# Kernel optimization log

Hardware: AMD Instinct MI355X
Metric: run time of the kernel (lower is better)

Reference implementation:

```python
import jax, jax.numpy as jnp
import numpy as np

LATENT_DIM = 16
POLY_ORDER = 3

# static index sets matching the ordering of the torch loops
_PAIR_I, _PAIR_J = np.triu_indices(LATENT_DIM)  # i<=j, row-major over i then j
_TRIPLES = np.array([(i, j, k)
                     for i in range(LATENT_DIM)
                     for j in range(i, LATENT_DIM)
                     for k in range(j, LATENT_DIM)], dtype=np.int32)
_TRI_I, _TRI_J, _TRI_K = _TRIPLES[:, 0], _TRIPLES[:, 1], _TRIPLES[:, 2]


def compute_library_order1(z):
    """Vectorized SINDy polynomial library: [1, z_i, z_i z_j (i<=j), z_i z_j z_k (i<=j<=k)]."""
    n = z.shape[0]
    ones = jnp.ones((n, 1), dtype=z.dtype)
    pairs = z[:, _PAIR_I] * z[:, _PAIR_J]                      # [N, 136]
    triples = z[:, _TRI_I] * z[:, _TRI_J] * z[:, _TRI_K]       # [N, 816]
    return jnp.concatenate([ones, z, pairs, triples], axis=1)  # [N, 969]


def setup_inputs() -> dict:
    key = jax.random.key(0)
    k1, k2 = jax.random.split(key)
    N = 262144
    library_dim = 1 + LATENT_DIM + _PAIR_I.shape[0] + _TRIPLES.shape[0]  # 969
    num_ode = 16
    z = jax.random.normal(k1, (N, LATENT_DIM), dtype=jnp.float32)
    coefficients = jax.random.normal(k2, (library_dim, num_ode), dtype=jnp.float32)
    coefficient_mask = jnp.ones((library_dim, num_ode), dtype=jnp.float32)
    return {"z": z, "coefficients": coefficients, "coefficient_mask": coefficient_mask}


def reference(z, coefficients, coefficient_mask):
    theta = compute_library_order1(z)                      # [N, 969]
    masked_coefficients = coefficients * coefficient_mask  # [969, 16]
    z_dot_pred = theta @ masked_coefficients               # [N, 16]
    l1_reg_loss = jnp.mean(jnp.abs(masked_coefficients))
    return (z_dot_pred, l1_reg_loss)
```

## Files before the change

### kernel.cpp

```cpp
#include <hip/hip_runtime.h>
#include <hip/hip_bf16.h>


#define LIB    969
#define NSLOT  248
#define NCHUNK 31
#define NROWS  262144
#define NOUT   16
#define BTAB_U4 1984

typedef __attribute__((ext_vector_type(8))) short bf16x8;
typedef __attribute__((ext_vector_type(4))) float f32x4;

struct Maps {
  unsigned char a[NSLOT], b[NSLOT], c[NSLOT];
  short l[NSLOT][4];
};

constexpr Maps build_maps() {
  Maps M{};
  int n = 0;
  M.a[n] = 16; M.b[n] = 16; M.c[n] = 16;
  M.l[n][0] = 0; M.l[n][1] = -1; M.l[n][2] = -1; M.l[n][3] = -1; n++;
  for (int a0 = 0; a0 < 4; a0++) {
    M.a[n] = (unsigned char)a0; M.b[n] = 16; M.c[n] = 16;
    for (int g = 0; g < 4; g++) M.l[n][g] = (short)(1 + ((a0 + 4 * g) & 15));
    n++;
  }
  bool pv[16][16] = {};
  for (int i = 0; i < 16; i++)
    for (int j = i; j < 16; j++) {
      if (pv[i][j]) continue;
      M.a[n] = (unsigned char)i; M.b[n] = (unsigned char)j; M.c[n] = 16;
      int mi[4], mj[4];
      for (int g = 0; g < 4; g++) {
        int x = (i + 4 * g) & 15, y = (j + 4 * g) & 15;
        int lo = x < y ? x : y, hi = x < y ? y : x;
        mi[g] = lo; mj[g] = hi; pv[lo][hi] = true;
      }
      for (int g = 0; g < 4; g++) {
        bool dup = false;
        for (int h = 0; h < g; h++) if (mi[h] == mi[g] && mj[h] == mj[g]) dup = true;
        M.l[n][g] = dup ? (short)-1
                        : (short)(17 + mi[g] * 16 - mi[g] * (mi[g] - 1) / 2 + (mj[g] - mi[g]));
      }
      n++;
    }
  bool tv[16][16][16] = {};
  for (int i = 0; i < 16; i++)
    for (int j = i; j < 16; j++)
      for (int k = j; k < 16; k++) {
        if (tv[i][j][k]) continue;
        M.a[n] = (unsigned char)i; M.b[n] = (unsigned char)j; M.c[n] = (unsigned char)k;
        int ti[4], tj[4], tk[4];
        for (int g = 0; g < 4; g++) {
          int x = (i + 4 * g) & 15, y = (j + 4 * g) & 15, w = (k + 4 * g) & 15, t;
          if (x > y) { t = x; x = y; y = t; }
          if (y > w) { t = y; y = w; w = t; }
          if (x > y) { t = x; x = y; y = t; }
          ti[g] = x; tj[g] = y; tk[g] = w; tv[x][y][w] = true;
        }
        for (int g = 0; g < 4; g++) {
          bool dup = false;
          for (int h = 0; h < g; h++)
            if (ti[h] == ti[g] && tj[h] == tj[g] && tk[h] == tk[g]) dup = true;
          if (dup) { M.l[n][g] = -1; continue; }
          int i2 = ti[g], j2 = tj[g], k2 = tk[g];
          int base = 0;
          for (int a2 = 0; a2 < i2; a2++) base += (16 - a2) * (17 - a2) / 2;
          int off = (j2 - i2) * (16 - i2) - (j2 - i2) * (j2 - i2 - 1) / 2 + (k2 - j2);
          M.l[n][g] = (short)(153 + base + off);
        }
        n++;
      }
  for (; n < NSLOT; n++) {
    M.a[n] = 16; M.b[n] = 16; M.c[n] = 16;
    M.l[n][0] = M.l[n][1] = M.l[n][2] = M.l[n][3] = -1;
  }
  return M;
}
constexpr Maps MP = build_maps();

__device__ inline unsigned short f2bf(float x) {
  unsigned int u = __builtin_bit_cast(unsigned int, x);
  u += 0x7fffu + ((u >> 16) & 1u);
  return (unsigned short)(u >> 16);
}
__global__ __launch_bounds__(256) void prep_kernel(const float* __restrict__ C,
                                                   const float* __restrict__ M,
                                                   unsigned short* __restrict__ Cb,
                                                   float* __restrict__ acc) {
  const int idx = blockIdx.x * 256 + threadIdx.x;
  const int s = idx >> 6, g = (idx >> 4) & 3, o = idx & 15;
  const int li = MP.l[s][g];
  float v = 0.f;
  if (li >= 0) v = C[li * 16 + o] * M[li * 16 + o];
  Cb[(((s >> 3) * 4 + g) * 16 + o) * 8 + (s & 7)] = f2bf(v);
  float t = fabsf(v);
  #pragma unroll
  for (int off = 32; off > 0; off >>= 1) t += __shfl_down(t, off);
  if ((threadIdx.x & 63) == 0) atomicAdd(acc, t);
}

__global__ __launch_bounds__(256) void sindy_kernel(const float* __restrict__ z,
                                                    const unsigned short* __restrict__ Cb,
                                                    const float* __restrict__ acc,
                                                    float* __restrict__ out) {
  __shared__ uint4 Blds[BTAB_U4];
  const int lane = threadIdx.x & 63;
  const int g = lane >> 4;
  const int o = lane & 15;
  const int rowBase = blockIdx.x * 64 + (threadIdx.x >> 6) * 16;
  const int r = rowBase + o;

  float z17[17];
  {
    const float4* z4 = (const float4*)z;
    #pragma unroll
    for (int c4 = 0; c4 < 4; c4++) {
      float4 v = z4[r * 4 + c4];
      z17[c4 * 4 + 0] = v.x; z17[c4 * 4 + 1] = v.y;
      z17[c4 * 4 + 2] = v.z; z17[c4 * 4 + 3] = v.w;
    }
    z17[16] = 1.0f;
  }

  {
    const uint4* src = (const uint4*)Cb;
    #pragma unroll
    for (int i = 0; i < 8; i++) {
      int e = i * 256 + threadIdx.x;
      if (e < BTAB_U4) Blds[e] = src[e];
    }
  }
  __syncthreads();

  const bool b0 = (g & 1) != 0, b1 = (g & 2) != 0;
  float t16[16], zr[17];
  #pragma unroll
  for (int m = 0; m < 16; m++) t16[m] = b0 ? z17[(m + 4) & 15] : z17[m];
  #pragma unroll
  for (int m = 0; m < 16; m++) zr[m] = b1 ? t16[(m + 8) & 15] : t16[m];
  zr[16] = 1.0f;

  const char* bbase = (const char*)Blds + lane * 16;

  f32x4 acc4 = {0.f, 0.f, 0.f, 0.f};
  #pragma unroll
  for (int c = 0; c < NCHUNK; c++) {
    bf16x8 af;
    #pragma unroll
    for (int m = 0; m < 8; m++) {
      const int s = c * 8 + m;
      float th = (zr[MP.a[s]] * zr[MP.b[s]]) * zr[MP.c[s]];
      __hip_bfloat16 h = __float2bfloat16(th);
      unsigned short u; __builtin_memcpy(&u, &h, 2);
      af[m] = (short)u;
    }
    bf16x8 bfrag = *(const bf16x8*)(bbase + c * 1024);
    acc4 = __builtin_amdgcn_mfma_f32_16x16x32_bf16(af, bfrag, acc4, 0, 0, 0);
  }

  #pragma unroll
  for (int p = 0; p < 4; p++)
    out[(rowBase + 4 * g + p) * 16 + o] = acc4[p];

  if (blockIdx.x == 0 && threadIdx.x == 0)
    out[NROWS * NOUT] = acc[0] * (1.0f / 15504.0f);
}

extern "C" void kernel_launch(void* const* d_in, const int* in_sizes, int n_in,
                              void* d_out, int out_size, void* d_ws, size_t ws_size,
                              hipStream_t stream) {
  const float* z = (const float*)d_in[0];
  const float* C = (const float*)d_in[1];
  const float* M = (const float*)d_in[2];
  float* out = (float*)d_out;
  float* acc = (float*)d_ws;
  unsigned short* Cb = (unsigned short*)((char*)d_ws + 64);

  (void)hipMemsetAsync(d_ws, 0, 4, stream);
  prep_kernel<<<NSLOT * 4 * 16 / 256, 256, 0, stream>>>(C, M, Cb, acc);
  sindy_kernel<<<NROWS / 64, 256, 0, stream>>>(z, Cb, acc, out);
}
```

Baseline: 56.00 us.

## Persistent-ish waves with z prefetch, fp16 MFMA, and memset-free L1 reduction

Removes the hipMemsetAsync and the atomic by having one extra block of the prep kernel compute the L1 mean directly into the output. Each wave now processes four 16-row tiles with software prefetch of the next z tile, which amortizes the LDS coefficient-table load over more rows using a 1024-block grid. Theta values are packed with cvt_pkrtz into fp16 and fed to the f16 MFMA instead of bf16 with manual rounding, cutting conversion instructions. The fp16 path may overflow for large cubic terms and uses round-toward-zero, which changes accuracy.

Measured after the change: 58.11 us. +3.8%, slower.

```diff
diff --git a/kernel.cpp b/kernel.cpp
--- a/kernel.cpp
+++ b/kernel.cpp
@@ -8,9 +8,12 @@
 #define NROWS  262144
 #define NOUT   16
 #define BTAB_U4 1984
-
-typedef __attribute__((ext_vector_type(8))) short bf16x8;
-typedef __attribute__((ext_vector_type(4))) float f32x4;
+#define TPW    4
+#define NBLK   1024
+
+typedef _Float16 f16x8 __attribute__((ext_vector_type(8)));
+typedef __fp16   h16x2 __attribute__((ext_vector_type(2)));
+typedef float    f32x4 __attribute__((ext_vector_type(4)));
 
 struct Maps {
   unsigned char a[NSLOT], b[NSLOT], c[NSLOT];
@@ -32,7 +35,7 @@
     for (int j = i; j < 16; j++) {
       if (pv[i][j]) continue;
       M.a[n] = (unsigned char)i; M.b[n] = (unsigned char)j; M.c[n] = 16;
-      int mi[4], mj[4];
+      int mi[4] = {}, mj[4] = {};
       for (int g = 0; g < 4; g++) {
         int x = (i + 4 * g) & 15, y = (j + 4 * g) & 15;
         int lo = x < y ? x : y, hi = x < y ? y : x;
@@ -52,9 +55,9 @@
       for (int k = j; k < 16; k++) {
         if (tv[i][j][k]) continue;
         M.a[n] = (unsigned char)i; M.b[n] = (unsigned char)j; M.c[n] = (unsigned char)k;
-        int ti[4], tj[4], tk[4];
+        int ti[4] = {}, tj[4] = {}, tk[4] = {};
         for (int g = 0; g < 4; g++) {
-          int x = (i + 4 * g) & 15, y = (j + 4 * g) & 15, w = (k + 4 * g) & 15, t;
+          int x = (i + 4 * g) & 15, y = (j + 4 * g) & 15, w = (k + 4 * g) & 15, t = 0;
           if (x > y) { t = x; x = y; y = t; }
           if (y > w) { t = y; y = w; w = t; }
           if (x > y) { t = x; x = y; y = t; }
@@ -81,92 +84,107 @@
 }
 constexpr Maps MP = build_maps();
 
-__device__ inline unsigned short f2bf(float x) {
-  unsigned int u = __builtin_bit_cast(unsigned int, x);
-  u += 0x7fffu + ((u >> 16) & 1u);
-  return (unsigned short)(u >> 16);
-}
 __global__ __launch_bounds__(256) void prep_kernel(const float* __restrict__ C,
                                                    const float* __restrict__ M,
                                                    unsigned short* __restrict__ Cb,
-                                                   float* __restrict__ acc) {
-  const int idx = blockIdx.x * 256 + threadIdx.x;
-  const int s = idx >> 6, g = (idx >> 4) & 3, o = idx & 15;
-  const int li = MP.l[s][g];
-  float v = 0.f;
-  if (li >= 0) v = C[li * 16 + o] * M[li * 16 + o];
-  Cb[(((s >> 3) * 4 + g) * 16 + o) * 8 + (s & 7)] = f2bf(v);
-  float t = fabsf(v);
-  #pragma unroll
-  for (int off = 32; off > 0; off >>= 1) t += __shfl_down(t, off);
-  if ((threadIdx.x & 63) == 0) atomicAdd(acc, t);
-}
-
-__global__ __launch_bounds__(256) void sindy_kernel(const float* __restrict__ z,
-                                                    const unsigned short* __restrict__ Cb,
-                                                    const float* __restrict__ acc,
-                                                    float* __restrict__ out) {
+                                                   float* __restrict__ out) {
+  if (blockIdx.x < 62) {
+    const int idx = blockIdx.x * 256 + threadIdx.x;
+    const int s = idx >> 6, g = (idx >> 4) & 3, o = idx & 15;
+    const int li = MP.l[s][g];
+    float v = 0.f;
+    if (li >= 0) v = C[li * 16 + o] * M[li * 16 + o];
+    _Float16 h = (_Float16)v;
+    unsigned short u; __builtin_memcpy(&u, &h, 2);
+    Cb[(((s >> 3) * 4 + g) * 16 + o) * 8 + (s & 7)] = u;
+  } else {
+    __shared__ float part[4];
+    float t = 0.f;
+    for (int i = threadIdx.x; i < LIB * 16; i += 256) t += fabsf(C[i] * M[i]);
+    #pragma unroll
+    for (int off = 32; off > 0; off >>= 1) t += __shfl_down(t, off);
+    if ((threadIdx.x & 63) == 0) part[threadIdx.x >> 6] = t;
+    __syncthreads();
+    if (threadIdx.x == 0)
+      out[NROWS * NOUT] = (part[0] + part[1] + part[2] + part[3]) * (1.0f / 15504.0f);
+  }
+}
+
+__global__ __launch_bounds__(256, 4) void sindy_kernel(const float* __restrict__ z,
+                                                       const unsigned short* __restrict__ Cb,
+                                                       float* __restrict__ out) {
   __shared__ uint4 Blds[BTAB_U4];
+  {
+    const uint4* src = (const uint4*)Cb;
+    #pragma unroll
+    for (int i = 0; i < 8; i++) {
+      int e = i * 256 + threadIdx.x;
+      if (e < BTAB_U4) Blds[e] = src[e];
+    }
+  }
+
   const int lane = threadIdx.x & 63;
   const int g = lane >> 4;
   const int o = lane & 15;
-  const int rowBase = blockIdx.x * 64 + (threadIdx.x >> 6) * 16;
-  const int r = rowBase + o;
-
-  float z17[17];
+  const int wid = blockIdx.x * 4 + (threadIdx.x >> 6);
+  const bool b0 = (g & 1) != 0, b1 = (g & 2) != 0;
+  const char* bbase = (const char*)Blds + lane * 16;
+
+  float4 zn[4];
   {
     const float4* z4 = (const float4*)z;
+    const int r = wid * TPW * 16 + o;
+    #pragma unroll
+    for (int c4 = 0; c4 < 4; c4++) zn[c4] = z4[r * 4 + c4];
+  }
+  __syncthreads();
+
+  int t = wid * TPW;
+  #pragma unroll
+  for (int k = 0; k < TPW; ++k, ++t) {
+    float z17[17];
     #pragma unroll
     for (int c4 = 0; c4 < 4; c4++) {
-      float4 v = z4[r * 4 + c4];
-      z17[c4 * 4 + 0] = v.x; z17[c4 * 4 + 1] = v.y;
-      z17[c4 * 4 + 2] = v.z; z17[c4 * 4 + 3] = v.w;
+      z17[c4 * 4 + 0] = zn[c4].x; z17[c4 * 4 + 1] = zn[c4].y;
+      z17[c4 * 4 + 2] = zn[c4].z; z17[c4 * 4 + 3] = zn[c4].w;
     }
     z17[16] = 1.0f;
-  }
-
-  {
-    const uint4* src = (const uint4*)Cb;
-    #pragma unroll
-    for (int i = 0; i < 8; i++) {
-      int e = i * 256 + threadIdx.x;
-      if (e < BTAB_U4) Blds[e] = src[e];
-    }
-  }
-  __syncthreads();
-
-  const bool b0 = (g & 1) != 0, b1 = (g & 2) != 0;
-  float t16[16], zr[17];
-  #pragma unroll
-  for (int m = 0; m < 16; m++) t16[m] = b0 ? z17[(m + 4) & 15] : z17[m];
-  #pragma unroll
-  for (int m = 0; m < 16; m++) zr[m] = b1 ? t16[(m + 8) & 15] : t16[m];
-  zr[16] = 1.0f;
-
-  const char* bbase = (const char*)Blds + lane * 16;
-
-  f32x4 acc4 = {0.f, 0.f, 0.f, 0.f};
-  #pragma unroll
-  for (int c = 0; c < NCHUNK; c++) {
-    bf16x8 af;
-    #pragma unroll
-    for (int m = 0; m < 8; m++) {
-      const int s = c * 8 + m;
-      float th = (zr[MP.a[s]] * zr[MP.b[s]]) * zr[MP.c[s]];
-      __hip_bfloat16 h = __float2bfloat16(th);
-      unsigned short u; __builtin_memcpy(&u, &h, 2);
-      af[m] = (short)u;
-    }
-    bf16x8 bfrag = *(const bf16x8*)(bbase + c * 1024);
-    acc4 = __builtin_amdgcn_mfma_f32_16x16x32_bf16(af, bfrag, acc4, 0, 0, 0);
-  }
-
-  #pragma unroll
-  for (int p = 0; p < 4; p++)
-    out[(rowBase + 4 * g + p) * 16 + o] = acc4[p];
-
-  if (blockIdx.x == 0 && threadIdx.x == 0)
-    out[NROWS * NOUT] = acc[0] * (1.0f / 15504.0f);
+    if (k + 1 < TPW) {
+      const float4* z4 = (const float4*)z;
+      const int r = (t + 1) * 16 + o;
+      #pragma unroll
+      for (int c4 = 0; c4 < 4; c4++) zn[c4] = z4[r * 4 + c4];
+    }
+    float t16[16], zr[17];
+    #pragma unroll
+    for (int m = 0; m < 16; m++) t16[m] = b0 ? z17[(m + 4) & 15] : z17[m];
+    #pragma unroll
+    for (int m = 0; m < 16; m++) zr[m] = b1 ? t16[(m + 8) & 15] : t16[m];
+    zr[16] = 1.0f;
+
+    f32x4 acc4 = {0.f, 0.f, 0.f, 0.f};
+    #pragma unroll
+    for (int c = 0; c < NCHUNK; c++) {
+      float th[8];
+      #pragma unroll
+      for (int m = 0; m < 8; m++) {
+        const int s = c * 8 + m;
+        th[m] = (zr[MP.a[s]] * zr[MP.b[s]]) * zr[MP.c[s]];
+      }
+      uint4 pkw;
+      pkw.x = __builtin_bit_cast(unsigned int, __builtin_amdgcn_cvt_pkrtz(th[0], th[1]));
+      pkw.y = __builtin_bit_cast(unsigned int, __builtin_amdgcn_cvt_pkrtz(th[2], th[3]));
+      pkw.z = __builtin_bit_cast(unsigned int, __builtin_amdgcn_cvt_pkrtz(th[4], th[5]));
+      pkw.w = __builtin_bit_cast(unsigned int, __builtin_amdgcn_cvt_pkrtz(th[6], th[7]));
+      f16x8 af = __builtin_bit_cast(f16x8, pkw);
+      f16x8 bfrag = *(const f16x8*)(bbase + c * 1024);
+      acc4 = __builtin_amdgcn_mfma_f32_16x16x32_f16(af, bfrag, acc4, 0, 0, 0);
+    }
+
+    #pragma unroll
+    for (int p = 0; p < 4; p++)
+      out[(t * 16 + 4 * g + p) * 16 + o] = acc4[p];
+  }
 }
 
 extern "C" void kernel_launch(void* const* d_in, const int* in_sizes, int n_in,
@@ -176,10 +194,8 @@
   const float* C = (const float*)d_in[1];
   const float* M = (const float*)d_in[2];
   float* out = (float*)d_out;
-  float* acc = (float*)d_ws;
-  unsigned short* Cb = (unsigned short*)((char*)d_ws + 64);
-
-  (void)hipMemsetAsync(d_ws, 0, 4, stream);
-  prep_kernel<<<NSLOT * 4 * 16 / 256, 256, 0, stream>>>(C, M, Cb, acc);
-  sindy_kernel<<<NROWS / 64, 256, 0, stream>>>(z, Cb, acc, out);
-}
+  unsigned short* Cb = (unsigned short*)d_ws;
+
+  prep_kernel<<<63, 256, 0, stream>>>(C, M, Cb, out);
+  sindy_kernel<<<NBLK, 256, 0, stream>>>(z, Cb, out);
+}
```
